# Kernel tuning notes

Hardware: AMD Instinct MI355X
Metric: run time of the kernel (lower is better)

## Reference

```python
import jax, jax.numpy as jnp
import numpy as np

N = 100000   # nodes
E = 1000000  # edges
D = 64       # in_features
D_OUT = 64   # out_features


def setup_inputs() -> dict:
    key = jax.random.key(0)
    k1, k2, k3, k4, k5, k6 = jax.random.split(key, 6)
    h = jax.random.normal(k1, (N, D), dtype=jnp.float32)          # current node features ndata['h']
    i = jax.random.normal(k2, (N, D), dtype=jnp.float32)          # initial features ndata['i']
    edge_src = jax.random.randint(k3, (E,), 0, N, dtype=jnp.int32)
    edge_dst = jax.random.randint(k4, (E,), 0, N, dtype=jnp.int32)
    edge_w = jax.random.uniform(k5, (E,), dtype=jnp.float32)      # scalar edge weight edata['x']
    stdv = 1.0 / np.sqrt(D_OUT)
    weight = jax.random.uniform(k6, (2 * D, D_OUT), dtype=jnp.float32,
                                minval=-stdv, maxval=stdv)        # variant=True -> in = 2*D
    return {
        "h": h, "i": i, "weight": weight, "edge_w": edge_w,
        "lamda": jnp.float32(0.5), "alpha": jnp.float32(0.1),
        "edge_src": edge_src, "edge_dst": edge_dst, "layer_idx": 4,
    }


def reference(h, i, weight, edge_w, lamda, alpha, edge_src, edge_dst, layer_idx):
    # theta = min(1, log(lamda/layer_idx + 1))
    theta = jnp.minimum(jnp.float32(1.0), jnp.log(lamda / layer_idx + 1.0))
    # update_all(u_mul_e('h','x','m'), sum('m','h')): edge-weighted gather-scatter SpMM
    m = h[edge_src] * edge_w[:, None]                 # [E, D]
    h_agg = jax.ops.segment_sum(m, edge_dst, num_segments=h.shape[0])  # [N, D]
    # variant=True branch
    support = jnp.concatenate([h_agg, i], axis=1)     # [N, 2D]
    r = (1.0 - alpha) * h_agg + alpha * i             # [N, D]
    out = theta * (support @ weight) + (1.0 - theta) * r
    # residual=True
    out = out + i
    return out
```

## Files before the change

kernel.cpp:

```cpp
#include <hip/hip_runtime.h>
#include <hip/hip_fp16.h>
#include <math.h>


#define DFEAT 64
#define BINSZ 64
#define NBINS 2048
#define CAP   1024
#define GPAD  16
#define CHUNK 4096
#define EPT   8
#define TPB   512

#define ASTR  72

typedef unsigned long long u64;
typedef __attribute__((ext_vector_type(8))) _Float16 f16x8;
typedef __attribute__((ext_vector_type(4))) float f32x4;

__device__ inline unsigned h2u(__half2 h) {
    union { __half2 h; unsigned u; } c; c.h = h; return c.u;
}
__device__ inline __half2 u2h(unsigned u) {
    union { unsigned u; __half2 h; } c; c.u = u; return c.h;
}

__global__ __launch_bounds__(256) void convert_kernel(
    const float* __restrict__ h, const float* __restrict__ weight,
    ushort* __restrict__ h16, ushort* __restrict__ w16,
    int* __restrict__ gcur, int total4) {
    int gid = blockIdx.x * 256 + threadIdx.x;
    int nth = gridDim.x * 256;
    if (gid < NBINS * GPAD) gcur[gid] = 0;
    for (int i = gid; i < total4; i += nth) {
        float4 v = ((const float4*)h)[i];
        uint2 o;
        o.x = h2u(__floats2half2_rn(v.x, v.y));
        o.y = h2u(__floats2half2_rn(v.z, v.w));
        ((uint2*)h16)[i] = o;
    }
    if (gid < 8192) {
        int j = gid & 7, l = (gid >> 3) & 63, cs = gid >> 9;
        int c = cs >> 2, s = cs & 3, q = l >> 4, m = l & 15;
        w16[gid] = __half_as_ushort(
            __float2half_rn(weight[(s * 32 + q * 8 + j) * DFEAT + c * 16 + m]));
    }
}

__global__ __launch_bounds__(512) void bin_fill_kernel(
    const int* __restrict__ e_src, const int* __restrict__ e_dst,
    const float* __restrict__ e_w, int* __restrict__ gcur,
    u64* __restrict__ bucket, int E) {
    __shared__ u64 staging[CHUNK];
    __shared__ int hist[NBINS];
    __shared__ ushort offs[NBINS];
    __shared__ ushort gbase[NBINS];
    __shared__ int part[TPB];

    int tid = threadIdx.x;
    int e0 = blockIdx.x * CHUNK;
    int cc = min(CHUNK, E - e0);

    for (int i = tid; i < NBINS; i += TPB) hist[i] = 0;
    __syncthreads();

    int bn[EPT], r[EPT];
    u64 pk[EPT];
#pragma unroll
    for (int j = 0; j < EPT; ++j) {
        int e = e0 + j * TPB + tid;
        bn[j] = -1;
        if (e < E) {
            int d = e_dst[e];
            int src = e_src[e];
            ushort wb = __half_as_ushort(__float2half_rn(e_w[e]));
            bn[j] = d >> 6;
            pk[j] = ((u64)wb << 48) | ((u64)(unsigned)bn[j] << 23) |
                    ((u64)(unsigned)(d & 63) << 17) | (u64)(unsigned)src;
        }
    }
#pragma unroll
    for (int j = 0; j < EPT; ++j)
        if (bn[j] >= 0) r[j] = atomicAdd(&hist[bn[j]], 1);
    __syncthreads();

    int c0 = hist[4 * tid], c1 = hist[4 * tid + 1];
    int c2 = hist[4 * tid + 2], c3 = hist[4 * tid + 3];
    int sum = c0 + c1 + c2 + c3;
    part[tid] = sum;
    __syncthreads();
    for (int ofs = 1; ofs < TPB; ofs <<= 1) {
        int t = (tid >= ofs) ? part[tid - ofs] : 0;
        __syncthreads();
        part[tid] += t;
        __syncthreads();
    }
    int excl = part[tid] - sum;
    offs[4 * tid] = (ushort)excl;
    offs[4 * tid + 1] = (ushort)(excl + c0);
    offs[4 * tid + 2] = (ushort)(excl + c0 + c1);
    offs[4 * tid + 3] = (ushort)(excl + c0 + c1 + c2);
    __syncthreads();

#pragma unroll
    for (int j = 0; j < EPT; ++j)
        if (bn[j] >= 0) staging[offs[bn[j]] + r[j]] = pk[j];

    for (int i = tid; i < NBINS; i += TPB) {
        int c = hist[i];
        int g = c ? atomicAdd(&gcur[i * GPAD], c) : 0;
        gbase[i] = (ushort)min(g, CAP);
    }
    __syncthreads();

#pragma unroll
    for (int j = 0; j < EPT; ++j) {
        int p = j * TPB + tid;
        if (p < cc) {
            u64 e = staging[p];
            int bin = (int)((e >> 23) & 2047);
            int pos = (int)gbase[bin] + (p - (int)offs[bin]);
            if (pos < CAP) {
                unsigned lo = (unsigned)(e & 0x1FFFF) |
                              (((unsigned)(e >> 17) & 63u) << 24);
                u64 hi = (e >> 48) << 32;
                bucket[(size_t)bin * CAP + pos] = hi | lo;
            }
        }
    }
}

__global__ __launch_bounds__(512) void spmm_kernel(
    const ushort* __restrict__ h16, const u64* __restrict__ bucket,
    const int* __restrict__ gcur, const ushort* __restrict__ w16,
    const float* __restrict__ ifeat,
    const float* __restrict__ lamda_p, const float* __restrict__ alpha_p,
    const int* __restrict__ layer_p,
    float* __restrict__ out, int N) {
    __shared__ u64 sorted[CAP];
    __shared__ __align__(16) ushort agg16[BINSZ * ASTR];
    __shared__ int hist[BINSZ], start[BINSZ];

    int tid = threadIdx.x;
    int bin = blockIdx.x;
    int base = bin << 6;
    int cnt = min(gcur[bin << 4], CAP);
    const u64* bk = bucket + (size_t)bin * CAP;

    if (tid < BINSZ) hist[tid] = 0;
    __syncthreads();

    u64 ev0 = 0, ev1 = 0;
    int dl0 = -1, dl1 = -1, r0 = 0, r1 = 0;
    if (tid < cnt) { ev0 = bk[tid]; dl0 = (int)((ev0 >> 24) & 63); }
    if (tid + TPB < cnt) { ev1 = bk[tid + TPB]; dl1 = (int)((ev1 >> 24) & 63); }
    if (dl0 >= 0) r0 = atomicAdd(&hist[dl0], 1);
    if (dl1 >= 0) r1 = atomicAdd(&hist[dl1], 1);
    __syncthreads();

    if (tid < 64) {
        int v = hist[tid];
        int s = v;
#pragma unroll
        for (int ofs = 1; ofs < 64; ofs <<= 1) {
            int t = __shfl_up(s, ofs);
            if (tid >= ofs) s += t;
        }
        start[tid] = s - v;
    }
    __syncthreads();

    if (dl0 >= 0) sorted[start[dl0] + r0] = ev0;
    if (dl1 >= 0) sorted[start[dl1] + r1] = ev1;
    if (cnt == 0 && tid == 0) sorted[0] = 0;
    __syncthreads();

    int lane = tid & 63, wv = tid >> 6;
    int g8 = lane >> 3;
    int m8 = lane & 7;
    int hf = g8 >> 2;
    int gs = g8 & 3;

    for (int kp = 0; kp < 4; ++kp) {
        int nl = (wv << 3) + (kp << 1) + hf;
        int d = hist[nl];
        int b0 = start[nl];
        int hi = (d > 0) ? (b0 + d - 1) : 0;
        __half2 a0 = u2h(0u), a1 = u2h(0u), a2 = u2h(0u), a3 = u2h(0u);
        for (int t0 = 0; t0 < d; t0 += 16) {
#pragma unroll
            for (int s = 0; s < 4; ++s) {
                int idx = t0 + (s << 2) + gs;
                u64 e = sorted[min(b0 + idx, hi)];
                ushort wb = (idx < d) ? (ushort)(e >> 32) : (ushort)0;
                __half2 w2 = __half2half2(__ushort_as_half(wb));
                unsigned src = ((unsigned)e) & 0xFFFFFFu;
                uint4 hv = *(const uint4*)(h16 + ((size_t)src << 6) + (m8 << 3));
                a0 = __hfma2(w2, u2h(hv.x), a0);
                a1 = __hfma2(w2, u2h(hv.y), a1);
                a2 = __hfma2(w2, u2h(hv.z), a2);
                a3 = __hfma2(w2, u2h(hv.w), a3);
            }
        }
        a0 = __hadd2(a0, u2h((unsigned)__shfl_xor((int)h2u(a0), 8)));
        a1 = __hadd2(a1, u2h((unsigned)__shfl_xor((int)h2u(a1), 8)));
        a2 = __hadd2(a2, u2h((unsigned)__shfl_xor((int)h2u(a2), 8)));
        a3 = __hadd2(a3, u2h((unsigned)__shfl_xor((int)h2u(a3), 8)));
        a0 = __hadd2(a0, u2h((unsigned)__shfl_xor((int)h2u(a0), 16)));
        a1 = __hadd2(a1, u2h((unsigned)__shfl_xor((int)h2u(a1), 16)));
        a2 = __hadd2(a2, u2h((unsigned)__shfl_xor((int)h2u(a2), 16)));
        a3 = __hadd2(a3, u2h((unsigned)__shfl_xor((int)h2u(a3), 16)));
        if (gs == 0) {
            uint4 o;
            o.x = h2u(a0); o.y = h2u(a1); o.z = h2u(a2); o.w = h2u(a3);
            *(uint4*)(agg16 + nl * ASTR + (m8 << 3)) = o;
        }
    }
    __syncthreads();

    float alf = alpha_p[0];
    float theta = fminf(1.0f, logf(lamda_p[0] / (float)layer_p[0] + 1.0f));
    int m = lane & 15, q = lane >> 4;
    int t = wv >> 1, ch = wv & 1;

    f16x8 faA[2], faI[2];
#pragma unroll
    for (int s = 0; s < 2; ++s)
        faA[s] = *(const f16x8*)(agg16 + (t * 16 + m) * ASTR + s * 32 + q * 8);
    {
        const float* ip = ifeat + (size_t)min(base + t * 16 + m, N - 1) * DFEAT;
#pragma unroll
        for (int s = 0; s < 2; ++s) {
            float4 v0 = *(const float4*)(ip + s * 32 + q * 8);
            float4 v1 = *(const float4*)(ip + s * 32 + q * 8 + 4);
            f16x8 tt;
            tt[0] = (_Float16)v0.x; tt[1] = (_Float16)v0.y;
            tt[2] = (_Float16)v0.z; tt[3] = (_Float16)v0.w;
            tt[4] = (_Float16)v1.x; tt[5] = (_Float16)v1.y;
            tt[6] = (_Float16)v1.z; tt[7] = (_Float16)v1.w;
            faI[s] = tt;
        }
    }

    f32x4 acc[2] = {{0.f, 0.f, 0.f, 0.f}, {0.f, 0.f, 0.f, 0.f}};
#pragma unroll
    for (int ci = 0; ci < 2; ++ci) {
        int c = ch * 2 + ci;
#pragma unroll
        for (int s = 0; s < 2; ++s) {
            f16x8 bA = *(const f16x8*)(w16 + ((c * 4 + s) * 64 + lane) * 8);
            acc[ci] = __builtin_amdgcn_mfma_f32_16x16x32_f16(faA[s], bA, acc[ci], 0, 0, 0);
            f16x8 bI = *(const f16x8*)(w16 + ((c * 4 + s + 2) * 64 + lane) * 8);
            acc[ci] = __builtin_amdgcn_mfma_f32_16x16x32_f16(faI[s], bI, acc[ci], 0, 0, 0);
        }
    }

#pragma unroll
    for (int ci = 0; ci < 2; ++ci) {
        int c = ch * 2 + ci;
        int col = c * 16 + m;
#pragma unroll
        for (int r = 0; r < 4; ++r) {
            int rowL = t * 16 + q * 4 + r;
            int row = base + rowL;
            if (row < N) {
                float av = __half2float(
                    *(const __half*)(agg16 + rowL * ASTR + col));
                float iv = ifeat[(size_t)row * DFEAT + col];
                out[(size_t)row * DFEAT + col] =
                    theta * acc[ci][r] +
                    (1.f - theta) * ((1.f - alf) * av + alf * iv) + iv;
            }
        }
    }
}

extern "C" void kernel_launch(void* const* d_in, const int* in_sizes, int n_in,
                              void* d_out, int out_size, void* d_ws, size_t ws_size,
                              hipStream_t stream) {
    const float* h       = (const float*)d_in[0];
    const float* ifeat   = (const float*)d_in[1];
    const float* weight  = (const float*)d_in[2];
    const float* edge_w  = (const float*)d_in[3];
    const float* lamda_p = (const float*)d_in[4];
    const float* alpha_p = (const float*)d_in[5];
    const int*   e_src   = (const int*)d_in[6];
    const int*   e_dst   = (const int*)d_in[7];
    const int*   layer_p = (const int*)d_in[8];
    float* out = (float*)d_out;

    int N = in_sizes[0] / DFEAT;
    int E = in_sizes[3];
    int nbins = (N + BINSZ - 1) >> 6;

    int* gcur = (int*)d_ws;
    u64* bucket = (u64*)((char*)d_ws + (size_t)NBINS * GPAD * sizeof(int));
    ushort* h16 = (ushort*)((char*)bucket + (size_t)NBINS * CAP * sizeof(u64));
    ushort* w16 = h16 + (size_t)N * DFEAT;

    int total4 = N * DFEAT / 4;
    convert_kernel<<<2048, 256, 0, stream>>>(h, weight, h16, w16, gcur, total4);

    bin_fill_kernel<<<(E + CHUNK - 1) / CHUNK, TPB, 0, stream>>>(
        e_src, e_dst, edge_w, gcur, bucket, E);

    spmm_kernel<<<nbins, TPB, 0, stream>>>(
        h16, bucket, gcur, w16, ifeat, lamda_p, alpha_p, layer_p, out, N);
}
```

Before: 164.6 us.

## Double destination bin size to 128 nodes and interleave gather loops across nodes

Bins now cover 128 destination nodes with 2048-entry capacity, halving the bin count and doubling the SpMM block to 1024 threads. The bucket packing, local scan and offsets widen to match. The gather loop now processes the four nodes per wave together, keeping independent accumulators so more h16 row loads are in flight at once. The ifeat load is hoisted before the gather. The cost is more registers and shared memory per block, fewer blocks to schedule, and 64-bit packing changes.

```diff
diff --git a/kernel.cpp b/kernel.cpp
--- a/kernel.cpp
+++ b/kernel.cpp
@@ -4,13 +4,14 @@
 
 
 #define DFEAT 64
-#define BINSZ 64
-#define NBINS 2048
-#define CAP   1024
+#define BINSZ 128
+#define NBINS 1024
+#define CAP   2048
 #define GPAD  16
 #define CHUNK 4096
 #define EPT   8
 #define TPB   512
+#define SPB   1024
 
 #define ASTR  72
 
@@ -53,15 +54,15 @@
     u64* __restrict__ bucket, int E) {
     __shared__ u64 staging[CHUNK];
     __shared__ int hist[NBINS];
-    __shared__ ushort offs[NBINS];
-    __shared__ ushort gbase[NBINS];
+    __shared__ int offs[NBINS];
+    __shared__ int gbase[NBINS];
     __shared__ int part[TPB];
 
     int tid = threadIdx.x;
     int e0 = blockIdx.x * CHUNK;
     int cc = min(CHUNK, E - e0);
 
-    for (int i = tid; i < NBINS; i += TPB) hist[i] = 0;
+    hist[tid] = 0; hist[tid + 512] = 0;
     __syncthreads();
 
     int bn[EPT], r[EPT];
@@ -74,9 +75,9 @@
             int d = e_dst[e];
             int src = e_src[e];
             ushort wb = __half_as_ushort(__float2half_rn(e_w[e]));
-            bn[j] = d >> 6;
-            pk[j] = ((u64)wb << 48) | ((u64)(unsigned)bn[j] << 23) |
-                    ((u64)(unsigned)(d & 63) << 17) | (u64)(unsigned)src;
+            bn[j] = d >> 7;
+            pk[j] = ((u64)wb << 48) | ((u64)(unsigned)bn[j] << 33) |
+                    ((u64)(unsigned)(d & 127) << 24) | (u64)(unsigned)src;
         }
     }
 #pragma unroll
@@ -84,10 +85,8 @@
         if (bn[j] >= 0) r[j] = atomicAdd(&hist[bn[j]], 1);
     __syncthreads();
 
-    int c0 = hist[4 * tid], c1 = hist[4 * tid + 1];
-    int c2 = hist[4 * tid + 2], c3 = hist[4 * tid + 3];
-    int sum = c0 + c1 + c2 + c3;
-    part[tid] = sum;
+    int a = hist[2 * tid], b = hist[2 * tid + 1];
+    part[tid] = a + b;
     __syncthreads();
     for (int ofs = 1; ofs < TPB; ofs <<= 1) {
         int t = (tid >= ofs) ? part[tid - ofs] : 0;
@@ -95,11 +94,9 @@
         part[tid] += t;
         __syncthreads();
     }
-    int excl = part[tid] - sum;
-    offs[4 * tid] = (ushort)excl;
-    offs[4 * tid + 1] = (ushort)(excl + c0);
-    offs[4 * tid + 2] = (ushort)(excl + c0 + c1);
-    offs[4 * tid + 3] = (ushort)(excl + c0 + c1 + c2);
+    int excl = part[tid] - (a + b);
+    offs[2 * tid] = excl;
+    offs[2 * tid + 1] = excl + a;
     __syncthreads();
 
 #pragma unroll
@@ -108,8 +105,7 @@
 
     for (int i = tid; i < NBINS; i += TPB) {
         int c = hist[i];
-        int g = c ? atomicAdd(&gcur[i * GPAD], c) : 0;
-        gbase[i] = (ushort)min(g, CAP);
+        gbase[i] = c ? atomicAdd(&gcur[i * GPAD], c) : 0;
     }
     __syncthreads();
 
@@ -118,19 +114,17 @@
         int p = j * TPB + tid;
         if (p < cc) {
             u64 e = staging[p];
-            int bin = (int)((e >> 23) & 2047);
-            int pos = (int)gbase[bin] + (p - (int)offs[bin]);
+            int bin = (int)((e >> 33) & 1023);
+            int pos = gbase[bin] + (p - offs[bin]);
             if (pos < CAP) {
-                unsigned lo = (unsigned)(e & 0x1FFFF) |
-                              (((unsigned)(e >> 17) & 63u) << 24);
-                u64 hi = (e >> 48) << 32;
-                bucket[(size_t)bin * CAP + pos] = hi | lo;
+                bucket[(size_t)bin * CAP + pos] =
+                    ((e >> 48) << 32) | (e & 0x7FFFFFFFull);
             }
         }
     }
 }
 
-__global__ __launch_bounds__(512) void spmm_kernel(
+__global__ __launch_bounds__(1024) void spmm_kernel(
     const ushort* __restrict__ h16, const u64* __restrict__ bucket,
     const int* __restrict__ gcur, const ushort* __restrict__ w16,
     const float* __restrict__ ifeat,
@@ -140,10 +134,11 @@
     __shared__ u64 sorted[CAP];
     __shared__ __align__(16) ushort agg16[BINSZ * ASTR];
     __shared__ int hist[BINSZ], start[BINSZ];
+    __shared__ int wsum[2];
 
     int tid = threadIdx.x;
     int bin = blockIdx.x;
-    int base = bin << 6;
+    int base = bin << 7;
     int cnt = min(gcur[bin << 4], CAP);
     const u64* bk = bucket + (size_t)bin * CAP;
 
@@ -152,22 +147,27 @@
 
     u64 ev0 = 0, ev1 = 0;
     int dl0 = -1, dl1 = -1, r0 = 0, r1 = 0;
-    if (tid < cnt) { ev0 = bk[tid]; dl0 = (int)((ev0 >> 24) & 63); }
-    if (tid + TPB < cnt) { ev1 = bk[tid + TPB]; dl1 = (int)((ev1 >> 24) & 63); }
+    if (tid < cnt) { ev0 = bk[tid]; dl0 = (int)((ev0 >> 24) & 127); }
+    if (tid + SPB < cnt) { ev1 = bk[tid + SPB]; dl1 = (int)((ev1 >> 24) & 127); }
     if (dl0 >= 0) r0 = atomicAdd(&hist[dl0], 1);
     if (dl1 >= 0) r1 = atomicAdd(&hist[dl1], 1);
     __syncthreads();
 
-    if (tid < 64) {
-        int v = hist[tid];
-        int s = v;
+    int lane = tid & 63, wv = tid >> 6;
+
+    int sv = 0, vv = 0;
+    if (tid < 128) {
+        vv = hist[tid];
+        sv = vv;
 #pragma unroll
         for (int ofs = 1; ofs < 64; ofs <<= 1) {
-            int t = __shfl_up(s, ofs);
-            if (tid >= ofs) s += t;
-        }
-        start[tid] = s - v;
-    }
+            int t = __shfl_up(sv, ofs);
+            if (lane >= ofs) sv += t;
+        }
+        if (lane == 63) wsum[tid >> 6] = sv;
+    }
+    __syncthreads();
+    if (tid < 128) start[tid] = sv - vv + ((tid >= 64) ? wsum[0] : 0);
     __syncthreads();
 
     if (dl0 >= 0) sorted[start[dl0] + r0] = ev0;
@@ -175,58 +175,14 @@
     if (cnt == 0 && tid == 0) sorted[0] = 0;
     __syncthreads();
 
-    int lane = tid & 63, wv = tid >> 6;
     int g8 = lane >> 3;
     int m8 = lane & 7;
     int hf = g8 >> 2;
     int gs = g8 & 3;
 
-    for (int kp = 0; kp < 4; ++kp) {
-        int nl = (wv << 3) + (kp << 1) + hf;
-        int d = hist[nl];
-        int b0 = start[nl];
-        int hi = (d > 0) ? (b0 + d - 1) : 0;
-        __half2 a0 = u2h(0u), a1 = u2h(0u), a2 = u2h(0u), a3 = u2h(0u);
-        for (int t0 = 0; t0 < d; t0 += 16) {
-#pragma unroll
-            for (int s = 0; s < 4; ++s) {
-                int idx = t0 + (s << 2) + gs;
-                u64 e = sorted[min(b0 + idx, hi)];
-                ushort wb = (idx < d) ? (ushort)(e >> 32) : (ushort)0;
-                __half2 w2 = __half2half2(__ushort_as_half(wb));
-                unsigned src = ((unsigned)e) & 0xFFFFFFu;
-                uint4 hv = *(const uint4*)(h16 + ((size_t)src << 6) + (m8 << 3));
-                a0 = __hfma2(w2, u2h(hv.x), a0);
-                a1 = __hfma2(w2, u2h(hv.y), a1);
-                a2 = __hfma2(w2, u2h(hv.z), a2);
-                a3 = __hfma2(w2, u2h(hv.w), a3);
-            }
-        }
-        a0 = __hadd2(a0, u2h((unsigned)__shfl_xor((int)h2u(a0), 8)));
-        a1 = __hadd2(a1, u2h((unsigned)__shfl_xor((int)h2u(a1), 8)));
-        a2 = __hadd2(a2, u2h((unsigned)__shfl_xor((int)h2u(a2), 8)));
-        a3 = __hadd2(a3, u2h((unsigned)__shfl_xor((int)h2u(a3), 8)));
-        a0 = __hadd2(a0, u2h((unsigned)__shfl_xor((int)h2u(a0), 16)));
-        a1 = __hadd2(a1, u2h((unsigned)__shfl_xor((int)h2u(a1), 16)));
-        a2 = __hadd2(a2, u2h((unsigned)__shfl_xor((int)h2u(a2), 16)));
-        a3 = __hadd2(a3, u2h((unsigned)__shfl_xor((int)h2u(a3), 16)));
-        if (gs == 0) {
-            uint4 o;
-            o.x = h2u(a0); o.y = h2u(a1); o.z = h2u(a2); o.w = h2u(a3);
-            *(uint4*)(agg16 + nl * ASTR + (m8 << 3)) = o;
-        }
-    }
-    __syncthreads();
-
-    float alf = alpha_p[0];
-    float theta = fminf(1.0f, logf(lamda_p[0] / (float)layer_p[0] + 1.0f));
     int m = lane & 15, q = lane >> 4;
     int t = wv >> 1, ch = wv & 1;
-
-    f16x8 faA[2], faI[2];
-#pragma unroll
-    for (int s = 0; s < 2; ++s)
-        faA[s] = *(const f16x8*)(agg16 + (t * 16 + m) * ASTR + s * 32 + q * 8);
+    f16x8 faI[2];
     {
         const float* ip = ifeat + (size_t)min(base + t * 16 + m, N - 1) * DFEAT;
 #pragma unroll
@@ -241,6 +197,69 @@
             faI[s] = tt;
         }
     }
+
+    int d_[4], b_[4], hi_[4];
+    int steps = 0;
+#pragma unroll
+    for (int kp = 0; kp < 4; ++kp) {
+        int nl = (wv << 3) + (kp << 1) + hf;
+        d_[kp] = hist[nl];
+        b_[kp] = start[nl];
+        hi_[kp] = (d_[kp] > 0) ? (b_[kp] + d_[kp] - 1) : 0;
+        steps = max(steps, (d_[kp] + 15) >> 4);
+    }
+    __half2 a0[4], a1[4], a2[4], a3[4];
+#pragma unroll
+    for (int kp = 0; kp < 4; ++kp) {
+        a0[kp] = u2h(0u); a1[kp] = u2h(0u);
+        a2[kp] = u2h(0u); a3[kp] = u2h(0u);
+    }
+    for (int st = 0; st < steps; ++st) {
+        int t0 = st << 4;
+#pragma unroll
+        for (int kp = 0; kp < 4; ++kp) {
+#pragma unroll
+            for (int s = 0; s < 4; ++s) {
+                int idx = t0 + (s << 2) + gs;
+                u64 e = sorted[min(b_[kp] + idx, hi_[kp])];
+                ushort wb = (idx < d_[kp]) ? (ushort)(e >> 32) : (ushort)0;
+                __half2 w2 = __half2half2(__ushort_as_half(wb));
+                unsigned src = ((unsigned)e) & 0xFFFFFFu;
+                uint4 hv = *(const uint4*)(h16 + ((size_t)src << 6) + (m8 << 3));
+                a0[kp] = __hfma2(w2, u2h(hv.x), a0[kp]);
+                a1[kp] = __hfma2(w2, u2h(hv.y), a1[kp]);
+                a2[kp] = __hfma2(w2, u2h(hv.z), a2[kp]);
+                a3[kp] = __hfma2(w2, u2h(hv.w), a3[kp]);
+            }
+        }
+    }
+#pragma unroll
+    for (int kp = 0; kp < 4; ++kp) {
+        __half2 x0 = a0[kp], x1 = a1[kp], x2 = a2[kp], x3 = a3[kp];
+        x0 = __hadd2(x0, u2h((unsigned)__shfl_xor((int)h2u(x0), 8)));
+        x1 = __hadd2(x1, u2h((unsigned)__shfl_xor((int)h2u(x1), 8)));
+        x2 = __hadd2(x2, u2h((unsigned)__shfl_xor((int)h2u(x2), 8)));
+        x3 = __hadd2(x3, u2h((unsigned)__shfl_xor((int)h2u(x3), 8)));
+        x0 = __hadd2(x0, u2h((unsigned)__shfl_xor((int)h2u(x0), 16)));
+        x1 = __hadd2(x1, u2h((unsigned)__shfl_xor((int)h2u(x1), 16)));
+        x2 = __hadd2(x2, u2h((unsigned)__shfl_xor((int)h2u(x2), 16)));
+        x3 = __hadd2(x3, u2h((unsigned)__shfl_xor((int)h2u(x3), 16)));
+        if (gs == 0) {
+            int nl = (wv << 3) + (kp << 1) + hf;
+            uint4 o;
+            o.x = h2u(x0); o.y = h2u(x1); o.z = h2u(x2); o.w = h2u(x3);
+            *(uint4*)(agg16 + nl * ASTR + (m8 << 3)) = o;
+        }
+    }
+    __syncthreads();
+
+    float alf = alpha_p[0];
+    float theta = fminf(1.0f, logf(lamda_p[0] / (float)layer_p[0] + 1.0f));
+
+    f16x8 faA[2];
+#pragma unroll
+    for (int s = 0; s < 2; ++s)
+        faA[s] = *(const f16x8*)(agg16 + (t * 16 + m) * ASTR + s * 32 + q * 8);
 
     f32x4 acc[2] = {{0.f, 0.f, 0.f, 0.f}, {0.f, 0.f, 0.f, 0.f}};
 #pragma unroll
@@ -291,7 +310,7 @@
 
     int N = in_sizes[0] / DFEAT;
     int E = in_sizes[3];
-    int nbins = (N + BINSZ - 1) >> 6;
+    int nbins = (N + BINSZ - 1) >> 7;
 
     int* gcur = (int*)d_ws;
     u64* bucket = (u64*)((char*)d_ws + (size_t)NBINS * GPAD * sizeof(int));
@@ -304,6 +323,6 @@
     bin_fill_kernel<<<(E + CHUNK - 1) / CHUNK, TPB, 0, stream>>>(
         e_src, e_dst, edge_w, gcur, bucket, E);
 
-    spmm_kernel<<<nbins, TPB, 0, stream>>>(
+    spmm_kernel<<<nbins, SPB, 0, stream>>>(
         h16, bucket, gcur, w16, ifeat, lamda_p, alpha_p, layer_p, out, N);
 }
```

After: 172.2 us. +4.6%, slower.

## Widen bin-fill blocks, use wave-shuffle scan, and prefetch initial features early

Applied to the files above, without the earlier changes.

The bin-fill kernel now runs 1024 threads per block with 4 edges per thread and replaces the barrier-heavy shared-memory prefix scan with a two-level wave shuffle scan. The global bucket atomics are moved ahead of the staging scatter, and the bucket packing is simplified so the spmm kernel decodes the bin-local destination at bit 17. The spmm kernel loads and converts the initial features before the gather loop so that load latency overlaps the aggregation. The gains are expected to be small, and the larger blocks and longer-lived registers could reduce occupancy.

```diff
diff --git a/kernel.cpp b/kernel.cpp
--- a/kernel.cpp
+++ b/kernel.cpp
@@ -9,7 +9,8 @@
 #define CAP   1024
 #define GPAD  16
 #define CHUNK 4096
-#define EPT   8
+#define BTPB  1024
+#define EPT   4
 #define TPB   512
 
 #define ASTR  72
@@ -47,7 +48,7 @@
     }
 }
 
-__global__ __launch_bounds__(512) void bin_fill_kernel(
+__global__ __launch_bounds__(1024) void bin_fill_kernel(
     const int* __restrict__ e_src, const int* __restrict__ e_dst,
     const float* __restrict__ e_w, int* __restrict__ gcur,
     u64* __restrict__ bucket, int E) {
@@ -55,20 +56,20 @@
     __shared__ int hist[NBINS];
     __shared__ ushort offs[NBINS];
     __shared__ ushort gbase[NBINS];
-    __shared__ int part[TPB];
+    __shared__ int wtot[16], wexcl[16];
 
     int tid = threadIdx.x;
     int e0 = blockIdx.x * CHUNK;
     int cc = min(CHUNK, E - e0);
 
-    for (int i = tid; i < NBINS; i += TPB) hist[i] = 0;
+    hist[tid] = 0; hist[tid + BTPB] = 0;
     __syncthreads();
 
     int bn[EPT], r[EPT];
     u64 pk[EPT];
 #pragma unroll
     for (int j = 0; j < EPT; ++j) {
-        int e = e0 + j * TPB + tid;
+        int e = e0 + j * BTPB + tid;
         bn[j] = -1;
         if (e < E) {
             int d = e_dst[e];
@@ -84,47 +85,53 @@
         if (bn[j] >= 0) r[j] = atomicAdd(&hist[bn[j]], 1);
     __syncthreads();
 
-    int c0 = hist[4 * tid], c1 = hist[4 * tid + 1];
-    int c2 = hist[4 * tid + 2], c3 = hist[4 * tid + 3];
-    int sum = c0 + c1 + c2 + c3;
-    part[tid] = sum;
-    __syncthreads();
-    for (int ofs = 1; ofs < TPB; ofs <<= 1) {
-        int t = (tid >= ofs) ? part[tid - ofs] : 0;
-        __syncthreads();
-        part[tid] += t;
-        __syncthreads();
-    }
-    int excl = part[tid] - sum;
-    offs[4 * tid] = (ushort)excl;
-    offs[4 * tid + 1] = (ushort)(excl + c0);
-    offs[4 * tid + 2] = (ushort)(excl + c0 + c1);
-    offs[4 * tid + 3] = (ushort)(excl + c0 + c1 + c2);
-    __syncthreads();
-
-#pragma unroll
-    for (int j = 0; j < EPT; ++j)
-        if (bn[j] >= 0) staging[offs[bn[j]] + r[j]] = pk[j];
-
-    for (int i = tid; i < NBINS; i += TPB) {
+    int lane = tid & 63, wv = tid >> 6;
+    int c0 = hist[2 * tid], c1 = hist[2 * tid + 1];
+    int sum = c0 + c1;
+    int s = sum;
+#pragma unroll
+    for (int ofs = 1; ofs < 64; ofs <<= 1) {
+        int t = __shfl_up(s, ofs);
+        if (lane >= ofs) s += t;
+    }
+    if (lane == 63) wtot[wv] = s;
+    __syncthreads();
+    if (tid < 16) {
+        int v = wtot[tid];
+        int sw = v;
+#pragma unroll
+        for (int ofs = 1; ofs < 16; ofs <<= 1) {
+            int t = __shfl_up(sw, ofs);
+            if (tid >= ofs) sw += t;
+        }
+        wexcl[tid] = sw - v;
+    }
+    __syncthreads();
+    int excl = wexcl[wv] + (s - sum);
+    offs[2 * tid] = (ushort)excl;
+    offs[2 * tid + 1] = (ushort)(excl + c0);
+    __syncthreads();
+
+    for (int i = tid; i < NBINS; i += BTPB) {
         int c = hist[i];
         int g = c ? atomicAdd(&gcur[i * GPAD], c) : 0;
         gbase[i] = (ushort)min(g, CAP);
     }
+#pragma unroll
+    for (int j = 0; j < EPT; ++j)
+        if (bn[j] >= 0) staging[offs[bn[j]] + r[j]] = pk[j];
     __syncthreads();
 
 #pragma unroll
     for (int j = 0; j < EPT; ++j) {
-        int p = j * TPB + tid;
+        int p = j * BTPB + tid;
         if (p < cc) {
             u64 e = staging[p];
             int bin = (int)((e >> 23) & 2047);
             int pos = (int)gbase[bin] + (p - (int)offs[bin]);
             if (pos < CAP) {
-                unsigned lo = (unsigned)(e & 0x1FFFF) |
-                              (((unsigned)(e >> 17) & 63u) << 24);
-                u64 hi = (e >> 48) << 32;
-                bucket[(size_t)bin * CAP + pos] = hi | lo;
+                bucket[(size_t)bin * CAP + pos] =
+                    ((e >> 48) << 32) | (e & 0x7FFFFF);
             }
         }
     }
@@ -152,8 +159,8 @@
 
     u64 ev0 = 0, ev1 = 0;
     int dl0 = -1, dl1 = -1, r0 = 0, r1 = 0;
-    if (tid < cnt) { ev0 = bk[tid]; dl0 = (int)((ev0 >> 24) & 63); }
-    if (tid + TPB < cnt) { ev1 = bk[tid + TPB]; dl1 = (int)((ev1 >> 24) & 63); }
+    if (tid < cnt) { ev0 = bk[tid]; dl0 = (int)((ev0 >> 17) & 63); }
+    if (tid + TPB < cnt) { ev1 = bk[tid + TPB]; dl1 = (int)((ev1 >> 17) & 63); }
     if (dl0 >= 0) r0 = atomicAdd(&hist[dl0], 1);
     if (dl1 >= 0) r1 = atomicAdd(&hist[dl1], 1);
     __syncthreads();
@@ -180,6 +187,24 @@
     int m8 = lane & 7;
     int hf = g8 >> 2;
     int gs = g8 & 3;
+
+    int m = lane & 15, q = lane >> 4;
+    int t = wv >> 1, ch = wv & 1;
+    f16x8 faI[2];
+    {
+        const float* ip = ifeat + (size_t)min(base + t * 16 + m, N - 1) * DFEAT;
+#pragma unroll
+        for (int s = 0; s < 2; ++s) {
+            float4 v0 = *(const float4*)(ip + s * 32 + q * 8);
+            float4 v1 = *(const float4*)(ip + s * 32 + q * 8 + 4);
+            f16x8 tt;
+            tt[0] = (_Float16)v0.x; tt[1] = (_Float16)v0.y;
+            tt[2] = (_Float16)v0.z; tt[3] = (_Float16)v0.w;
+            tt[4] = (_Float16)v1.x; tt[5] = (_Float16)v1.y;
+            tt[6] = (_Float16)v1.z; tt[7] = (_Float16)v1.w;
+            faI[s] = tt;
+        }
+    }
 
     for (int kp = 0; kp < 4; ++kp) {
         int nl = (wv << 3) + (kp << 1) + hf;
@@ -194,7 +219,7 @@
                 u64 e = sorted[min(b0 + idx, hi)];
                 ushort wb = (idx < d) ? (ushort)(e >> 32) : (ushort)0;
                 __half2 w2 = __half2half2(__ushort_as_half(wb));
-                unsigned src = ((unsigned)e) & 0xFFFFFFu;
+                unsigned src = ((unsigned)e) & 0x1FFFFu;
                 uint4 hv = *(const uint4*)(h16 + ((size_t)src << 6) + (m8 << 3));
                 a0 = __hfma2(w2, u2h(hv.x), a0);
                 a1 = __hfma2(w2, u2h(hv.y), a1);
@@ -220,27 +245,11 @@
 
     float alf = alpha_p[0];
     float theta = fminf(1.0f, logf(lamda_p[0] / (float)layer_p[0] + 1.0f));
-    int m = lane & 15, q = lane >> 4;
-    int t = wv >> 1, ch = wv & 1;
-
-    f16x8 faA[2], faI[2];
+
+    f16x8 faA[2];
 #pragma unroll
     for (int s = 0; s < 2; ++s)
         faA[s] = *(const f16x8*)(agg16 + (t * 16 + m) * ASTR + s * 32 + q * 8);
-    {
-        const float* ip = ifeat + (size_t)min(base + t * 16 + m, N - 1) * DFEAT;
-#pragma unroll
-        for (int s = 0; s < 2; ++s) {
-            float4 v0 = *(const float4*)(ip + s * 32 + q * 8);
-            float4 v1 = *(const float4*)(ip + s * 32 + q * 8 + 4);
-            f16x8 tt;
-            tt[0] = (_Float16)v0.x; tt[1] = (_Float16)v0.y;
-            tt[2] = (_Float16)v0.z; tt[3] = (_Float16)v0.w;
-            tt[4] = (_Float16)v1.x; tt[5] = (_Float16)v1.y;
-            tt[6] = (_Float16)v1.z; tt[7] = (_Float16)v1.w;
-            faI[s] = tt;
-        }
-    }
 
     f32x4 acc[2] = {{0.f, 0.f, 0.f, 0.f}, {0.f, 0.f, 0.f, 0.f}};
 #pragma unroll
@@ -301,7 +310,7 @@
     int total4 = N * DFEAT / 4;
     convert_kernel<<<2048, 256, 0, stream>>>(h, weight, h16, w16, gcur, total4);
 
-    bin_fill_kernel<<<(E + CHUNK - 1) / CHUNK, TPB, 0, stream>>>(
+    bin_fill_kernel<<<(E + CHUNK - 1) / CHUNK, BTPB, 0, stream>>>(
         e_src, e_dst, edge_w, gcur, bucket, E);
 
     spmm_kernel<<<nbins, TPB, 0, stream>>>(
```

Result: no change. 163.4 us (-0.7%).
